# Kernel tuning notes

Hardware: AMD Instinct MI355X
Metric: run time of the kernel (lower is better)

## Reference

```python
import jax, jax.numpy as jnp
import numpy as np

N_NODES = 100000
N_EDGES = 400000
N_GRAPHS = 2000
IN_DIM = 58
HEADS = 4
HID = 64           # per-head hidden = output_dim // heads = 256 // 4
OUT = 256
NEG_SLOPE = 0.2    # PyG GATConv default


def _glorot(key, shape):
    fan_in, fan_out = shape[0], shape[-1]
    lim = jnp.sqrt(6.0 / (fan_in + fan_out)).astype(jnp.float32)
    return jax.random.uniform(key, shape, jnp.float32, -lim, lim)


def setup_inputs() -> dict:
    key = jax.random.key(0)
    ks = jax.random.split(key, 16)
    x = jax.random.normal(ks[0], (N_NODES, IN_DIM), jnp.float32)
    edge_index = jax.random.randint(ks[1], (2, N_EDGES), 0, N_NODES, jnp.int64)
    batch = jnp.sort(jax.random.randint(ks[2], (N_NODES,), 0, N_GRAPHS, jnp.int64))
    return {
        "x": x,
        "edge_index": edge_index,
        "batch": batch,
        # layer 1: 58 -> 4 heads x 64, concat -> 256
        "W1": _glorot(ks[3], (IN_DIM, HEADS * HID)),
        "a_src1": _glorot(ks[4], (HEADS, HID)),
        "a_dst1": _glorot(ks[5], (HEADS, HID)),
        "b1": jnp.zeros((HEADS * HID,), jnp.float32),
        # layer 2: 256 -> 4 heads x 64, concat -> 256
        "W2": _glorot(ks[6], (HEADS * HID, HEADS * HID)),
        "a_src2": _glorot(ks[7], (HEADS, HID)),
        "a_dst2": _glorot(ks[8], (HEADS, HID)),
        "b2": jnp.zeros((HEADS * HID,), jnp.float32),
        # layer 3: 256 -> 1 head x 256, no concat (mean over 1 head)
        "W3": _glorot(ks[9], (HEADS * HID, OUT)),
        "a_src3": _glorot(ks[10], (1, OUT)),
        "a_dst3": _glorot(ks[11], (1, OUT)),
        "b3": jnp.zeros((OUT,), jnp.float32),
    }


def _gat_layer(x, src, dst, W, a_src, a_dst, b, heads, ch, concat):
    n = x.shape[0]
    h = (x @ W).reshape(n, heads, ch)                      # [N,H,C]
    e_src = jnp.einsum("nhc,hc->nh", h, a_src)             # [N,H]
    e_dst = jnp.einsum("nhc,hc->nh", h, a_dst)
    e = jax.nn.leaky_relu(e_src[src] + e_dst[dst], NEG_SLOPE)  # [E,H]
    # segment softmax over destination nodes (self-loops ensure non-empty segments)
    m = jax.ops.segment_max(e, dst, num_segments=n)
    ex = jnp.exp(e - m[dst])
    denom = jax.ops.segment_sum(ex, dst, num_segments=n)
    coef = ex / denom[dst]                                 # [E,H]
    out = jax.ops.segment_sum(h[src] * coef[:, :, None], dst, num_segments=n)
    out = out.reshape(n, heads * ch) if concat else out.mean(axis=1)
    return out + b


def reference(x, edge_index, batch, W1, a_src1, a_dst1, b1,
              W2, a_src2, a_dst2, b2, W3, a_src3, a_dst3, b3):
    n = x.shape[0]
    loops = jnp.arange(n, dtype=edge_index.dtype)
    src = jnp.concatenate([edge_index[0], loops])          # add_self_loops (PyG default)
    dst = jnp.concatenate([edge_index[1], loops])
    h = jax.nn.relu(_gat_layer(x, src, dst, W1, a_src1, a_dst1, b1, HEADS, HID, True))
    h = jax.nn.relu(_gat_layer(h, src, dst, W2, a_src2, a_dst2, b2, HEADS, HID, True))
    h = _gat_layer(h, src, dst, W3, a_src3, a_dst3, b3, 1, OUT, False)
    # global max pool over graphs
    return jax.ops.segment_max(h, batch, num_segments=N_GRAPHS)
```

## Files before the change

### kernel.cpp

```cpp
#include <hip/hip_runtime.h>
#include <hip/hip_bf16.h>
#include <math.h>

#define N_NODES_C 100000
#define E_ORIG    400000
#define E_TOT     500000
#define N_GRAPHS_C 2000
#define KDIM      256

typedef __attribute__((ext_vector_type(8))) short short8v;
typedef __attribute__((ext_vector_type(4))) float f32x4;

__device__ __forceinline__ void gload_lds16(const void* g, void* l) {
    __builtin_amdgcn_global_load_lds(
        (const __attribute__((address_space(1))) unsigned int*)g,
        (__attribute__((address_space(3))) unsigned int*)l, 16, 0, 0);
}

__device__ __forceinline__ float bflo(unsigned u) { return __uint_as_float(u << 16); }
__device__ __forceinline__ float bfhi(unsigned u) { return __uint_as_float(u & 0xffff0000u); }

#define XE  (N_NODES_C * 64)
#define W1E (256 * 64)
#define WBE (256 * 256)
__global__ __launch_bounds__(256) void conv_all_count(
        const float* __restrict__ x, const float* __restrict__ W1,
        const float* __restrict__ W2, const float* __restrict__ W3,
        const int* __restrict__ ei,
        __hip_bfloat16* __restrict__ Xb, __hip_bfloat16* __restrict__ Wt1,
        __hip_bfloat16* __restrict__ Wt2, __hip_bfloat16* __restrict__ Wt3,
        int* __restrict__ deg) {
    int idx = blockIdx.x * 256 + threadIdx.x;
    if (idx < E_TOT) {
        int d = (idx < E_ORIG) ? ei[E_ORIG + idx] : (idx - E_ORIG);
        atomicAdd(&deg[d], 1);
    }
    if (idx < XE) {
        int row = idx >> 6, c = idx & 63;
        float v = (c < 58) ? x[row * 58 + c] : 0.f;
        Xb[idx] = __float2bfloat16(v);
    } else if (idx < XE + W1E) {
        int i = idx - XE;
        int c = i >> 6, k = i & 63;
        float v = (k < 58) ? W1[k * 256 + c] : 0.f;
        Wt1[i] = __float2bfloat16(v);
    } else if (idx < XE + W1E + WBE) {
        int i = idx - XE - W1E;
        int c = i >> 8, k = i & 255;
        Wt2[i] = __float2bfloat16(W2[k * 256 + c]);
    } else if (idx < XE + W1E + 2 * WBE) {
        int i = idx - XE - W1E - WBE;
        int c = i >> 8, k = i & 255;
        Wt3[i] = __float2bfloat16(W3[k * 256 + c]);
    }
}

__global__ void scan_chunk(const int* __restrict__ in, int* __restrict__ out,
                           int* __restrict__ partials, int n) {
    __shared__ int s[256];
    int tid = threadIdx.x;
    int i = blockIdx.x * 256 + tid;
    int v = (i < n) ? in[i] : 0;
    s[tid] = v;
    __syncthreads();
    for (int off = 1; off < 256; off <<= 1) {
        int t = (tid >= off) ? s[tid - off] : 0;
        __syncthreads();
        s[tid] += t;
        __syncthreads();
    }
    if (i < n) out[i] = s[tid] - v;
    if (tid == 255) partials[blockIdx.x] = s[255];
}

__global__ void scan_fix(int* __restrict__ rowoff, const int* __restrict__ partials, int n) {
    __shared__ int sred[256];
    int t = threadIdx.x;
    int acc = 0;
    for (int i = t; i < blockIdx.x; i += 256) acc += partials[i];
    sred[t] = acc;
    __syncthreads();
    for (int off = 128; off; off >>= 1) {
        if (t < off) sred[t] += sred[t + off];
        __syncthreads();
    }
    int base = sred[0];
    int i = blockIdx.x * 256 + t;
    if (i < n) rowoff[i] += base;
}

__global__ void scatter_k(const int* __restrict__ ei, const int* __restrict__ rowoff,
                          int* cursor, int* __restrict__ csr_src,
                          int* __restrict__ csr_dst) {
    int e = blockIdx.x * 256 + threadIdx.x;
    if (e >= E_TOT) return;
    int s, d;
    if (e < E_ORIG) { s = ei[e]; d = ei[E_ORIG + e]; }
    else            { s = e - E_ORIG; d = s; }
    int pos = rowoff[d] + atomicAdd(&cursor[d], 1);
    csr_src[pos] = s;
    csr_dst[pos] = d;
}

template <int KPAD, int NH>
__global__ __launch_bounds__(256, 2) void gemm_mfma(
        const __hip_bfloat16* __restrict__ Xb, const __hip_bfloat16* __restrict__ Wt,
        const float* __restrict__ ASRC, const float* __restrict__ ADST,
        __hip_bfloat16* __restrict__ H, float* __restrict__ ES, float* __restrict__ ED) {
    __shared__ char As[128 * 128];
    __shared__ char Bs[256 * 128];
    __shared__ float red[2][128][2];

    const int t = threadIdx.x;
    const int wv = t >> 6, lane = t & 63;
    const int wr = wv >> 1, wc = wv & 1;
    const int r15 = lane & 15, hi = lane >> 4;
    const int n0 = blockIdx.x * 128;
    const int srow = lane >> 3;
    const int sx = ((lane & 7) ^ srow) * 16;
    constexpr int KB = KPAD * 2;

    f32x4 acc[4][8];
#pragma unroll
    for (int m = 0; m < 4; m++)
#pragma unroll
        for (int n = 0; n < 8; n++) acc[m][n] = (f32x4){0.f, 0.f, 0.f, 0.f};

    for (int kt = 0; kt < KPAD / 64; kt++) {
        if (kt) __syncthreads();
        const int k0b = kt * 128;
#pragma unroll
        for (int p = 0; p < 4; p++) {
            int i = wv * 4 + p;
            int gr = n0 + i * 8 + srow;
            if (gr > N_NODES_C - 1) gr = N_NODES_C - 1;
            gload_lds16((const char*)Xb + (size_t)gr * KB + k0b + sx, As + i * 1024);
        }
#pragma unroll
        for (int p = 0; p < 8; p++) {
            int i = wv * 8 + p;
            int col = i * 8 + srow;
            gload_lds16((const char*)Wt + (size_t)col * KB + k0b + sx, Bs + i * 1024);
        }
        asm volatile("s_waitcnt vmcnt(0)" ::: "memory");
        __syncthreads();

#pragma unroll
        for (int ks = 0; ks < 2; ks++) {
            const int cx = ((ks * 4 + hi) ^ (r15 & 7)) * 16;
            short8v a[4];
#pragma unroll
            for (int m = 0; m < 4; m++)
                a[m] = *(const short8v*)(As + (wr * 64 + m * 16 + r15) * 128 + cx);
#pragma unroll
            for (int n = 0; n < 8; n++) {
                short8v b = *(const short8v*)(Bs + (wc * 128 + n * 16 + r15) * 128 + cx);
#pragma unroll
                for (int m = 0; m < 4; m++)
                    acc[m][n] = __builtin_amdgcn_mfma_f32_16x16x32_bf16(a[m], b, acc[m][n], 0, 0, 0);
            }
        }
    }

    float asv[8], adv[8];
#pragma unroll
    for (int n = 0; n < 8; n++) {
        int col = wc * 128 + n * 16 + r15;
        asv[n] = ASRC[col];
        adv[n] = ADST[col];
    }

#pragma unroll
    for (int m = 0; m < 4; m++) {
#pragma unroll
        for (int j = 0; j < 4; j++) {
            int lrow = wr * 64 + m * 16 + hi * 4 + j;
            int row = n0 + lrow;
            bool ok = row < N_NODES_C;
            if (ok) {
#pragma unroll
                for (int n = 0; n < 8; n++)
                    H[(size_t)row * KDIM + wc * 128 + n * 16 + r15] =
                        __float2bfloat16(acc[m][n][j]);
            }
            if (NH == 4) {
                float p0s = 0.f, p1s = 0.f, p0d = 0.f, p1d = 0.f;
#pragma unroll
                for (int n = 0; n < 4; n++) {
                    p0s = fmaf(acc[m][n][j], asv[n], p0s);
                    p0d = fmaf(acc[m][n][j], adv[n], p0d);
                    p1s = fmaf(acc[m][n + 4][j], asv[n + 4], p1s);
                    p1d = fmaf(acc[m][n + 4][j], adv[n + 4], p1d);
                }
#pragma unroll
                for (int s = 8; s; s >>= 1) {
                    p0s += __shfl_xor(p0s, s, 16);
                    p0d += __shfl_xor(p0d, s, 16);
                    p1s += __shfl_xor(p1s, s, 16);
                    p1d += __shfl_xor(p1d, s, 16);
                }
                if (r15 == 0 && ok) {
                    ES[row * 4 + wc * 2 + 0] = p0s;
                    ES[row * 4 + wc * 2 + 1] = p1s;
                    ED[row * 4 + wc * 2 + 0] = p0d;
                    ED[row * 4 + wc * 2 + 1] = p1d;
                }
            } else {
                float ps = 0.f, pd = 0.f;
#pragma unroll
                for (int n = 0; n < 8; n++) {
                    ps = fmaf(acc[m][n][j], asv[n], ps);
                    pd = fmaf(acc[m][n][j], adv[n], pd);
                }
#pragma unroll
                for (int s = 8; s; s >>= 1) {
                    ps += __shfl_xor(ps, s, 16);
                    pd += __shfl_xor(pd, s, 16);
                }
                if (r15 == 0) { red[0][lrow][wc] = ps; red[1][lrow][wc] = pd; }
            }
        }
    }
    if (NH == 1) {
        __syncthreads();
        if (t < 128) {
            int row = n0 + t;
            if (row < N_NODES_C) {
                ES[row] = red[0][t][0] + red[0][t][1];
                ED[row] = red[1][t][0] + red[1][t][1];
            }
        }
    }
}

#define ECAP 160
template <int NH, bool RELU>
__global__ __launch_bounds__(256) void agg_kernel(
        const __hip_bfloat16* __restrict__ H, const int* __restrict__ rowoff,
        const int* __restrict__ csr_src, const int* __restrict__ csr_dst,
        const float* __restrict__ ES, const float* __restrict__ ED,
        const float* __restrict__ bias, __hip_bfloat16* __restrict__ Out) {
    __shared__ float Els[ECAP * NH];
    __shared__ int   Sls[ECAP];
    __shared__ int   roff[9];
    int t = threadIdx.x;
    int n0 = blockIdx.x * 8;
    if (t < 9) roff[t] = rowoff[n0 + t];
    __syncthreads();
    int beg0 = roff[0];
    int ne = roff[8] - beg0;
    int nl = (ne < ECAP) ? ne : ECAP;
    for (int j = t; j < nl; j += 256) {
        int slot = beg0 + j;
        int srcj = csr_src[slot];
        int dj   = csr_dst[slot];
        Sls[j] = srcj;
        if (NH == 4) {
            float4 es = *(const float4*)&ES[srcj * 4];
            float4 ed = *(const float4*)&ED[dj * 4];
            float e;
            e = es.x + ed.x; Els[j * 4 + 0] = (e > 0.f) ? e : 0.2f * e;
            e = es.y + ed.y; Els[j * 4 + 1] = (e > 0.f) ? e : 0.2f * e;
            e = es.z + ed.z; Els[j * 4 + 2] = (e > 0.f) ? e : 0.2f * e;
            e = es.w + ed.w; Els[j * 4 + 3] = (e > 0.f) ? e : 0.2f * e;
        } else {
            float e = ES[srcj] + ED[dj];
            Els[j] = (e > 0.f) ? e : 0.2f * e;
        }
    }
    __syncthreads();

    int g = t >> 5;
    int node = n0 + g;
    int l = t & 31;
    int c0 = l * 8;
    int head = (NH == 4) ? (l >> 3) : 0;
    int jb = roff[g] - beg0, je = roff[g + 1] - beg0;
    int jeF = (je < ECAP) ? je : ECAP;

    float m = -1e30f;
    for (int j = jb; j < jeF; j++) m = fmaxf(m, Els[j * NH + head]);
    if (je > ECAP) {
        float edv = ED[node * NH + head];
        for (int j = ECAP; j < je; j++) {
            float e = ES[csr_src[beg0 + j] * NH + head] + edv;
            e = (e > 0.f) ? e : 0.2f * e;
            m = fmaxf(m, e);
        }
    }

    float s = 0.f;
    float a[8];
#pragma unroll
    for (int i = 0; i < 8; i++) a[i] = 0.f;
    const unsigned short* Hu = (const unsigned short*)H;

#define ACC8(v, p) \
    a[0] = fmaf(p, bflo(v.x), a[0]); a[1] = fmaf(p, bfhi(v.x), a[1]); \
    a[2] = fmaf(p, bflo(v.y), a[2]); a[3] = fmaf(p, bfhi(v.y), a[3]); \
    a[4] = fmaf(p, bflo(v.z), a[4]); a[5] = fmaf(p, bfhi(v.z), a[5]); \
    a[6] = fmaf(p, bflo(v.w), a[6]); a[7] = fmaf(p, bfhi(v.w), a[7]);

    int j = jb;
    for (; j + 4 <= jeF; j += 4) {
        int s0 = Sls[j], s1 = Sls[j + 1], s2 = Sls[j + 2], s3 = Sls[j + 3];
        float e0 = Els[(j + 0) * NH + head], e1 = Els[(j + 1) * NH + head];
        float e2 = Els[(j + 2) * NH + head], e3 = Els[(j + 3) * NH + head];
        uint4 v0 = *(const uint4*)(Hu + (size_t)s0 * KDIM + c0);
        uint4 v1 = *(const uint4*)(Hu + (size_t)s1 * KDIM + c0);
        uint4 v2 = *(const uint4*)(Hu + (size_t)s2 * KDIM + c0);
        uint4 v3 = *(const uint4*)(Hu + (size_t)s3 * KDIM + c0);
        float p0 = __expf(e0 - m), p1 = __expf(e1 - m);
        float p2 = __expf(e2 - m), p3 = __expf(e3 - m);
        s += p0 + p1 + p2 + p3;
        ACC8(v0, p0)
        ACC8(v1, p1)
        ACC8(v2, p2)
        ACC8(v3, p3)
    }
    for (; j < jeF; j++) {
        int s0 = Sls[j];
        float e0 = Els[j * NH + head];
        uint4 v0 = *(const uint4*)(Hu + (size_t)s0 * KDIM + c0);
        float p0 = __expf(e0 - m);
        s += p0;
        ACC8(v0, p0)
    }
    if (je > ECAP) {
        float edv = ED[node * NH + head];
        for (int jj = ECAP; jj < je; jj++) {
            int sj = csr_src[beg0 + jj];
            float e = ES[sj * NH + head] + edv;
            e = (e > 0.f) ? e : 0.2f * e;
            float p = __expf(e - m);
            s += p;
            uint4 v = *(const uint4*)(Hu + (size_t)sj * KDIM + c0);
            ACC8(v, p)
        }
    }
#undef ACC8

    float inv = 1.f / s;
    float4 b0 = *(const float4*)&bias[c0];
    float4 b1 = *(const float4*)&bias[c0 + 4];
    float o[8];
    o[0] = fmaf(a[0], inv, b0.x); o[1] = fmaf(a[1], inv, b0.y);
    o[2] = fmaf(a[2], inv, b0.z); o[3] = fmaf(a[3], inv, b0.w);
    o[4] = fmaf(a[4], inv, b1.x); o[5] = fmaf(a[5], inv, b1.y);
    o[6] = fmaf(a[6], inv, b1.z); o[7] = fmaf(a[7], inv, b1.w);
    __hip_bfloat16 rb[8];
#pragma unroll
    for (int i = 0; i < 8; i++) {
        float v = RELU ? fmaxf(o[i], 0.f) : o[i];
        rb[i] = __float2bfloat16(v);
    }
    *(uint4*)&Out[(size_t)node * KDIM + c0] = *(uint4*)rb;
}

__global__ __launch_bounds__(256) void pool_k(
        const __hip_bfloat16* __restrict__ O, const int* __restrict__ batch,
        float* __restrict__ out) {
    __shared__ int range[2];
    __shared__ float red[3][256];
    int g = blockIdx.x, k = threadIdx.x;
    if (k < 2) {
        int v = g + k;
        int lo = 0, hi = N_NODES_C;
        while (lo < hi) { int mid = (lo + hi) >> 1; if (batch[mid] < v) lo = mid + 1; else hi = mid; }
        range[k] = lo;
    }
    __syncthreads();
    int cg = k & 63;
    int ro = k >> 6;
    float m0 = -INFINITY, m1 = -INFINITY, m2 = -INFINITY, m3 = -INFINITY;
    const unsigned short* Ou = (const unsigned short*)O;
    for (int i = range[0] + ro; i < range[1]; i += 4) {
        uint2 v = *(const uint2*)(Ou + (size_t)i * KDIM + cg * 4);
        m0 = fmaxf(m0, bflo(v.x)); m1 = fmaxf(m1, bfhi(v.x));
        m2 = fmaxf(m2, bflo(v.y)); m3 = fmaxf(m3, bfhi(v.y));
    }
    if (ro) {
        red[ro - 1][cg * 4 + 0] = m0; red[ro - 1][cg * 4 + 1] = m1;
        red[ro - 1][cg * 4 + 2] = m2; red[ro - 1][cg * 4 + 3] = m3;
    }
    __syncthreads();
    if (ro == 0) {
        m0 = fmaxf(fmaxf(m0, red[0][cg * 4 + 0]), fmaxf(red[1][cg * 4 + 0], red[2][cg * 4 + 0]));
        m1 = fmaxf(fmaxf(m1, red[0][cg * 4 + 1]), fmaxf(red[1][cg * 4 + 1], red[2][cg * 4 + 1]));
        m2 = fmaxf(fmaxf(m2, red[0][cg * 4 + 2]), fmaxf(red[1][cg * 4 + 2], red[2][cg * 4 + 2]));
        m3 = fmaxf(fmaxf(m3, red[0][cg * 4 + 3]), fmaxf(red[1][cg * 4 + 3], red[2][cg * 4 + 3]));
        float4 o = make_float4(m0, m1, m2, m3);
        *(float4*)&out[(size_t)g * KDIM + cg * 4] = o;
    }
}

extern "C" void kernel_launch(void* const* d_in, const int* in_sizes, int n_in,
                              void* d_out, int out_size, void* d_ws, size_t ws_size,
                              hipStream_t stream) {
    const float* x     = (const float*)d_in[0];
    const int*   ei    = (const int*)d_in[1];
    const int*   batch = (const int*)d_in[2];
    const float* W1  = (const float*)d_in[3];
    const float* as1 = (const float*)d_in[4];
    const float* ad1 = (const float*)d_in[5];
    const float* b1  = (const float*)d_in[6];
    const float* W2  = (const float*)d_in[7];
    const float* as2 = (const float*)d_in[8];
    const float* ad2 = (const float*)d_in[9];
    const float* b2  = (const float*)d_in[10];
    const float* W3  = (const float*)d_in[11];
    const float* as3 = (const float*)d_in[12];
    const float* ad3 = (const float*)d_in[13];
    const float* b3  = (const float*)d_in[14];
    float* out = (float*)d_out;

    char* p = (char*)d_ws;
    auto alloc = [&](size_t bytes) { char* r = p; p += (bytes + 255) & ~(size_t)255; return r; };
    __hip_bfloat16* Xb  = (__hip_bfloat16*)alloc((size_t)N_NODES_C * 64 * 2);
    __hip_bfloat16* Hb  = (__hip_bfloat16*)alloc((size_t)N_NODES_C * KDIM * 2);
    __hip_bfloat16* Nb  = (__hip_bfloat16*)alloc((size_t)N_NODES_C * KDIM * 2);
    __hip_bfloat16* Wt1 = (__hip_bfloat16*)alloc(256 * 64 * 2);
    __hip_bfloat16* Wt2 = (__hip_bfloat16*)alloc(256 * 256 * 2);
    __hip_bfloat16* Wt3 = (__hip_bfloat16*)alloc(256 * 256 * 2);
    float* ES     = (float*)alloc((size_t)N_NODES_C * 4 * 4);
    float* ED     = (float*)alloc((size_t)N_NODES_C * 4 * 4);
    int* degcur   = (int*)alloc((size_t)(2 * N_NODES_C + 1) * 4);
    int* deg      = degcur;
    int* cursor   = degcur + (N_NODES_C + 1);
    int* rowoff   = (int*)alloc((N_NODES_C + 1) * 4);
    int* csr      = (int*)alloc((size_t)E_TOT * 4 + 256);
    int* csrd     = (int*)alloc((size_t)E_TOT * 4);
    int* partials = (int*)alloc(512 * 4);

    hipMemsetAsync(degcur, 0, (size_t)(2 * N_NODES_C + 1) * 4, stream);
    int ctot = XE + W1E + 2 * WBE;
    conv_all_count<<<(ctot + 255) / 256, 256, 0, stream>>>(
        x, W1, W2, W3, ei, Xb, Wt1, Wt2, Wt3, deg);

    int nb = (N_NODES_C + 1 + 255) / 256;
    scan_chunk<<<nb, 256, 0, stream>>>(deg, rowoff, partials, N_NODES_C + 1);
    scan_fix<<<nb, 256, 0, stream>>>(rowoff, partials, N_NODES_C + 1);
    int egrid = (E_TOT + 255) / 256;
    scatter_k<<<egrid, 256, 0, stream>>>(ei, rowoff, cursor, csr, csrd);

    int ggrid = (N_NODES_C + 127) / 128;
    int agrid = N_NODES_C / 8;
    gemm_mfma<64, 4><<<ggrid, 256, 0, stream>>>(Xb, Wt1, as1, ad1, Hb, ES, ED);
    agg_kernel<4, true><<<agrid, 256, 0, stream>>>(Hb, rowoff, csr, csrd, ES, ED, b1, Nb);
    gemm_mfma<256, 4><<<ggrid, 256, 0, stream>>>(Nb, Wt2, as2, ad2, Hb, ES, ED);
    agg_kernel<4, true><<<agrid, 256, 0, stream>>>(Hb, rowoff, csr, csrd, ES, ED, b2, Nb);
    gemm_mfma<256, 1><<<ggrid, 256, 0, stream>>>(Nb, Wt3, as3, ad3, Hb, ES, ED);
    agg_kernel<1, false><<<agrid, 256, 0, stream>>>(Hb, rowoff, csr, csrd, ES, ED, b3, Nb);
    pool_k<<<N_GRAPHS_C, 256, 0, stream>>>(Nb, batch, out);
}
```

Before: 318.1 us.

## Double-buffer GEMM LDS tiles with smaller 64-row blocks and nontemporal agg stores

The MFMA GEMM block tile shrinks from 128 to 64 rows, which doubles the grid and halves the accumulator registers. The LDS A/B tiles become double-buffered so the next K-slice's global-to-LDS loads are issued before computing on the current one. The separate reduction buffer is dropped in favour of reusing the A tile. The aggregation kernel's output store becomes nontemporal. The trade-off is that B (weight) tiles are now reloaded twice as often across the grid, and the loop relies on the barrier alone rather than an explicit vmcnt wait, which may not guarantee the async LDS loads have completed.

Result: slower. 345.9 us (+8.7%).

```diff
diff --git a/kernel.cpp b/kernel.cpp
--- a/kernel.cpp
+++ b/kernel.cpp
@@ -10,6 +10,7 @@
 
 typedef __attribute__((ext_vector_type(8))) short short8v;
 typedef __attribute__((ext_vector_type(4))) float f32x4;
+typedef __attribute__((ext_vector_type(4))) unsigned int u32x4;
 
 __device__ __forceinline__ void gload_lds16(const void* g, void* l) {
     __builtin_amdgcn_global_load_lds(
@@ -103,61 +104,62 @@
 }
 
 template <int KPAD, int NH>
-__global__ __launch_bounds__(256, 2) void gemm_mfma(
+__global__ __launch_bounds__(256) void gemm_mfma(
         const __hip_bfloat16* __restrict__ Xb, const __hip_bfloat16* __restrict__ Wt,
         const float* __restrict__ ASRC, const float* __restrict__ ADST,
         __hip_bfloat16* __restrict__ H, float* __restrict__ ES, float* __restrict__ ED) {
-    __shared__ char As[128 * 128];
-    __shared__ char Bs[256 * 128];
-    __shared__ float red[2][128][2];
+    __shared__ char As[2][64 * 128];
+    __shared__ char Bs[2][256 * 128];
 
     const int t = threadIdx.x;
     const int wv = t >> 6, lane = t & 63;
     const int wr = wv >> 1, wc = wv & 1;
     const int r15 = lane & 15, hi = lane >> 4;
-    const int n0 = blockIdx.x * 128;
+    const int n0 = blockIdx.x * 64;
     const int srow = lane >> 3;
     const int sx = ((lane & 7) ^ srow) * 16;
     constexpr int KB = KPAD * 2;
-
-    f32x4 acc[4][8];
-#pragma unroll
-    for (int m = 0; m < 4; m++)
+    constexpr int NT = KPAD / 64;
+
+    f32x4 acc[2][8];
+#pragma unroll
+    for (int m = 0; m < 2; m++)
 #pragma unroll
         for (int n = 0; n < 8; n++) acc[m][n] = (f32x4){0.f, 0.f, 0.f, 0.f};
 
-    for (int kt = 0; kt < KPAD / 64; kt++) {
-        if (kt) __syncthreads();
+    auto stage = [&](int b, int kt) {
         const int k0b = kt * 128;
 #pragma unroll
-        for (int p = 0; p < 4; p++) {
-            int i = wv * 4 + p;
+        for (int p = 0; p < 2; p++) {
+            int i = wv * 2 + p;
             int gr = n0 + i * 8 + srow;
             if (gr > N_NODES_C - 1) gr = N_NODES_C - 1;
-            gload_lds16((const char*)Xb + (size_t)gr * KB + k0b + sx, As + i * 1024);
+            gload_lds16((const char*)Xb + (size_t)gr * KB + k0b + sx, As[b] + i * 1024);
         }
 #pragma unroll
         for (int p = 0; p < 8; p++) {
             int i = wv * 8 + p;
             int col = i * 8 + srow;
-            gload_lds16((const char*)Wt + (size_t)col * KB + k0b + sx, Bs + i * 1024);
-        }
-        asm volatile("s_waitcnt vmcnt(0)" ::: "memory");
+            gload_lds16((const char*)Wt + (size_t)col * KB + k0b + sx, Bs[b] + i * 1024);
+        }
+    };
+
+    stage(0, 0);
+    for (int kt = 0; kt < NT; kt++) {
         __syncthreads();
-
+        if (kt + 1 < NT) stage((kt + 1) & 1, kt + 1);
+        const char* Ab = As[kt & 1];
+        const char* Bb = Bs[kt & 1];
 #pragma unroll
         for (int ks = 0; ks < 2; ks++) {
             const int cx = ((ks * 4 + hi) ^ (r15 & 7)) * 16;
-            short8v a[4];
-#pragma unroll
-            for (int m = 0; m < 4; m++)
-                a[m] = *(const short8v*)(As + (wr * 64 + m * 16 + r15) * 128 + cx);
+            short8v a0 = *(const short8v*)(Ab + (wr * 32 + 0  + r15) * 128 + cx);
+            short8v a1 = *(const short8v*)(Ab + (wr * 32 + 16 + r15) * 128 + cx);
 #pragma unroll
             for (int n = 0; n < 8; n++) {
-                short8v b = *(const short8v*)(Bs + (wc * 128 + n * 16 + r15) * 128 + cx);
-#pragma unroll
-                for (int m = 0; m < 4; m++)
-                    acc[m][n] = __builtin_amdgcn_mfma_f32_16x16x32_bf16(a[m], b, acc[m][n], 0, 0, 0);
+                short8v b = *(const short8v*)(Bb + (wc * 128 + n * 16 + r15) * 128 + cx);
+                acc[0][n] = __builtin_amdgcn_mfma_f32_16x16x32_bf16(a0, b, acc[0][n], 0, 0, 0);
+                acc[1][n] = __builtin_amdgcn_mfma_f32_16x16x32_bf16(a1, b, acc[1][n], 0, 0, 0);
             }
         }
     }
@@ -169,12 +171,14 @@
         asv[n] = ASRC[col];
         adv[n] = ADST[col];
     }
-
-#pragma unroll
-    for (int m = 0; m < 4; m++) {
+    float* red = (float*)As;
+    if (NH == 1) __syncthreads();
+
+#pragma unroll
+    for (int m = 0; m < 2; m++) {
 #pragma unroll
         for (int j = 0; j < 4; j++) {
-            int lrow = wr * 64 + m * 16 + hi * 4 + j;
+            int lrow = wr * 32 + m * 16 + hi * 4 + j;
             int row = n0 + lrow;
             bool ok = row < N_NODES_C;
             if (ok) {
@@ -217,17 +221,20 @@
                     ps += __shfl_xor(ps, s, 16);
                     pd += __shfl_xor(pd, s, 16);
                 }
-                if (r15 == 0) { red[0][lrow][wc] = ps; red[1][lrow][wc] = pd; }
+                if (r15 == 0) {
+                    red[(0 * 64 + lrow) * 2 + wc] = ps;
+                    red[(1 * 64 + lrow) * 2 + wc] = pd;
+                }
             }
         }
     }
     if (NH == 1) {
         __syncthreads();
-        if (t < 128) {
+        if (t < 64) {
             int row = n0 + t;
             if (row < N_NODES_C) {
-                ES[row] = red[0][t][0] + red[0][t][1];
-                ED[row] = red[1][t][0] + red[1][t][1];
+                ES[row] = red[(0 * 64 + t) * 2 + 0] + red[(0 * 64 + t) * 2 + 1];
+                ED[row] = red[(1 * 64 + t) * 2 + 0] + red[(1 * 64 + t) * 2 + 1];
             }
         }
     }
@@ -354,7 +361,7 @@
         float v = RELU ? fmaxf(o[i], 0.f) : o[i];
         rb[i] = __float2bfloat16(v);
     }
-    *(uint4*)&Out[(size_t)node * KDIM + c0] = *(uint4*)rb;
+    __builtin_nontemporal_store(*(u32x4*)rb, (u32x4*)&Out[(size_t)node * KDIM + c0]);
 }
 
 __global__ __launch_bounds__(256) void pool_k(
@@ -443,7 +450,7 @@
     int egrid = (E_TOT + 255) / 256;
     scatter_k<<<egrid, 256, 0, stream>>>(ei, rowoff, cursor, csr, csrd);
 
-    int ggrid = (N_NODES_C + 127) / 128;
+    int ggrid = (N_NODES_C + 63) / 64;
     int agrid = N_NODES_C / 8;
     gemm_mfma<64, 4><<<ggrid, 256, 0, stream>>>(Xb, Wt1, as1, ad1, Hb, ES, ED);
     agg_kernel<4, true><<<agrid, 256, 0, stream>>>(Hb, rowoff, csr, csrd, ES, ED, b1, Nb);
```
